# Kernel tuning notes

Measured on AMD Instinct MI355X. Metric: run time of the kernel, lower is better.

The kernel has to match this reference:

```python
import jax, jax.numpy as jnp
import numpy as np
from jax import lax

# geomloss SamplesLoss('sinkhorn', p=2, blur=0.01, scaling=0.9) semantics:
# debiased Sinkhorn divergence S_eps(a,b) = OT_eps(x,y) - 0.5*OT_eps(x,x) - 0.5*OT_eps(y,y)
# with cost C = ||x-y||^2 / 2, uniform weights, and epsilon annealing from
# diameter^p down to blur^p with ratio scaling^p.
P = 2
BLUR = 0.01
SCALING = 0.9
DIAMETER = 8.0  # static upper bound on point-cloud spread for randn data

def _eps_schedule():
    scales = []
    s = DIAMETER
    while s > BLUR:
        scales.append(s)
        s *= SCALING
    scales.append(BLUR)
    return jnp.asarray(np.array(scales, np.float32) ** P)

def _sqcost(x, y):
    # x: [B,N,D], y: [B,M,D] -> C[B,N,M] = 0.5*||x_i-y_j||^2
    x2 = jnp.sum(x * x, -1)[:, :, None]
    y2 = jnp.sum(y * y, -1)[:, None, :]
    return 0.5 * (x2 + y2 - 2.0 * jnp.einsum('bnd,bmd->bnm', x, y))

def _sinkhorn_divergence(x, y):
    B, N, _ = x.shape
    M = y.shape[1]
    logN = jnp.log(jnp.float32(N))
    logM = jnp.log(jnp.float32(M))
    eps_list = _eps_schedule()

    Cxy = _sqcost(x, y)          # [B,N,M]
    Cyx = jnp.swapaxes(Cxy, 1, 2)
    Cxx = _sqcost(x, x)
    Cyy = _sqcost(y, y)

    def softmin(eps, C, h, logw):
        # -eps * log sum_j exp(log w_j + (h_j - C_ij)/eps)
        return -eps * jax.nn.logsumexp((h[:, None, :] - C) / eps - logw, axis=-1)

    # potentials computed under envelope theorem (no grad through iterations)
    Cxy_d, Cyx_d = lax.stop_gradient(Cxy), lax.stop_gradient(Cyx)
    Cxx_d, Cyy_d = lax.stop_gradient(Cxx), lax.stop_gradient(Cyy)

    z = jnp.zeros((B, N), x.dtype)
    zy = jnp.zeros((B, M), x.dtype)

    def body(carry, eps):
        f, g, fx, gy = carry
        ft = softmin(eps, Cxy_d, g, logM)
        gt = softmin(eps, Cyx_d, f, logN)
        f, g = 0.5 * (f + ft), 0.5 * (g + gt)
        fx = 0.5 * (fx + softmin(eps, Cxx_d, fx, logN))
        gy = 0.5 * (gy + softmin(eps, Cyy_d, gy, logM))
        return (f, g, fx, gy), None

    (f, g, fx, gy), _ = lax.scan(body, (z, zy, z, zy), eps_list)

    # last extrapolation at target eps, differentiable w.r.t. the costs
    eps_t = eps_list[-1]
    f_fin = softmin(eps_t, Cxy, lax.stop_gradient(g), logM)
    g_fin = softmin(eps_t, Cyx, lax.stop_gradient(f), logN)
    fx_fin = softmin(eps_t, Cxx, lax.stop_gradient(fx), logN)
    gy_fin = softmin(eps_t, Cyy, lax.stop_gradient(gy), logM)

    # S = <a, f - fx> + <b, g - gy>, uniform weights
    return jnp.mean(f_fin - fx_fin, axis=-1) + jnp.mean(g_fin - gy_fin, axis=-1)  # [B]


def setup_inputs() -> dict:
    key = jax.random.key(0)
    k1, k2 = jax.random.split(key)
    B, N, D = 8, 2048, 3
    p1 = jax.random.normal(k1, (B, N, D), dtype=jnp.float32)
    p2 = jax.random.normal(k2, (B, N, D), dtype=jnp.float32)
    return {"p1": p1, "p2": p2}


def reference(p1, p2):
    # EMD_Loss.forward: mean over batch of per-sample Sinkhorn divergences
    return jnp.mean(_sinkhorn_divergence(p1, p2))
```

## Files before the change

kernel.cpp:

```cpp
#include <hip/hip_runtime.h>
#include <math.h>

#define NPTS 2048
#define NB 8
#define R 4
#define NW 16
#define CCH 128

typedef float v2f __attribute__((ext_vector_type(2)));

__device__ __forceinline__ float wexp2(float v) { return __builtin_amdgcn_exp2f(v); }
__device__ __forceinline__ v2f fma2(v2f a, v2f b, v2f c) {
  return __builtin_elementwise_fma(a, b, c);
}
__device__ __forceinline__ v2f max2(v2f a, v2f b) {
  return __builtin_elementwise_max(a, b);
}

__global__ __launch_bounds__(256) void emd_init(const float* __restrict__ x,
                                                const float* __restrict__ y,
                                                float4* __restrict__ x4,
                                                float4* __restrict__ y4,
                                                float* __restrict__ pot0,
                                                float* __restrict__ out) {
  int t = blockIdx.x * blockDim.x + threadIdx.x;
  if (t < NB * NPTS) {
    float a0 = x[3 * t], a1 = x[3 * t + 1], a2 = x[3 * t + 2];
    x4[t] = make_float4(a0, a1, a2, 0.5f * (a0 * a0 + a1 * a1 + a2 * a2));
    float b0 = y[3 * t], b1 = y[3 * t + 1], b2 = y[3 * t + 2];
    y4[t] = make_float4(b0, b1, b2, 0.5f * (b0 * b0 + b1 * b1 + b2 * b2));
  }
  pot0[t] = 0.0f;
  if (t == 0) out[0] = 0.0f;
}

template <bool FINAL>
__global__ __launch_bounds__(1024, 4) void emd_sweep(const float4* __restrict__ x4,
                                                     const float4* __restrict__ y4,
                                                     const float* __restrict__ pot_in,
                                                     float* __restrict__ pot_out,
                                                     float* __restrict__ out,
                                                     float c,
                                                     float neg_eps_ln2,
                                                     float eps_logM) {
  __shared__ union {
    struct {
      float4 A[NPTS / 2];
      float4 B[NPTS / 2];
    } cp;
    struct {
      float m[NW][256];
      float l[NW][256];
    } mg;
  } sh;

  int blk = blockIdx.x;
  int mat = blk >> 6;
  int b = (blk >> 3) & 7;
  int rg = blk & 7;
  int tid = threadIdx.x;
  int lane = tid & 63;
  int w = tid >> 6;

  const float4* rowp = (mat == 1 || mat == 3) ? y4 : x4;
  const float4* colp = (mat == 0 || mat == 3) ? y4 : x4;
  int hidx = (mat < 2) ? (mat ^ 1) : mat;
  const float* h = pot_in + (hidx * NB + b) * NPTS;
  const float4* colb = colp + b * NPTS;

  {
    float4 q0 = colb[2 * tid];
    float4 q1 = colb[2 * tid + 1];
    float2 hv = ((const float2*)h)[tid];
    sh.cp.A[tid] = make_float4(q0.x, q1.x, q0.y, q1.y);
    sh.cp.B[tid] = make_float4(q0.z, q1.z, (hv.x - q0.w) * c, (hv.y - q1.w) * c);
  }
  __syncthreads();

  int rowbase = rg * 256;
  const float4* rowb = rowp + b * NPTS + rowbase;

  v2f xs0[R], xs1[R], xs2[R];
  float m[R], l[R];
#pragma unroll
  for (int r = 0; r < R; ++r) {
    float4 p = rowb[r * 64 + lane];
    float a0 = p.x * c, a1 = p.y * c, a2 = p.z * c;
    xs0[r] = (v2f){a0, a0};
    xs1[r] = (v2f){a1, a1};
    xs2[r] = (v2f){a2, a2};
    m[r] = -INFINITY;
    l[r] = 0.0f;
  }

  int p0 = w * (CCH / 2);
  for (int tp = 0; tp < CCH / 2; tp += 4) {
    float4 A[4], B[4];
#pragma unroll
    for (int j = 0; j < 4; ++j) {
      A[j] = sh.cp.A[p0 + tp + j];
      B[j] = sh.cp.B[p0 + tp + j];
    }
#pragma unroll
    for (int r = 0; r < R; ++r) {
      v2f s2[4];
#pragma unroll
      for (int j = 0; j < 4; ++j) {
        v2f qx = {A[j].x, A[j].y};
        v2f qy = {A[j].z, A[j].w};
        v2f qz = {B[j].x, B[j].y};
        v2f qw = {B[j].z, B[j].w};
        s2[j] = fma2(xs0[r], qx, fma2(xs1[r], qy, fma2(xs2[r], qz, qw)));
      }
      v2f t0 = max2(s2[0], s2[1]);
      v2f t1 = max2(s2[2], s2[3]);
      v2f u = max2(t0, t1);
      float mt = fmaxf(u.x, u.y);
      float mn = fmaxf(m[r], mt);
      v2f mn2 = {mn, mn};
      v2f acc = {0.0f, 0.0f};
#pragma unroll
      for (int j = 0; j < 4; ++j) {
        v2f d = s2[j] - mn2;
        v2f e;
        e.x = wexp2(d.x);
        e.y = wexp2(d.y);
        acc += e;
      }
      float er = wexp2(m[r] - mn);
      l[r] = fmaf(l[r], er, acc.x + acc.y);
      m[r] = mn;
    }
  }

  __syncthreads();
#pragma unroll
  for (int r = 0; r < R; ++r) {
    sh.mg.m[w][r * 64 + lane] = m[r];
    sh.mg.l[w][r * 64 + lane] = l[r];
  }
  __syncthreads();

  if (w < 4) {
    int row = w * 64 + lane;
    float M = sh.mg.m[0][row];
#pragma unroll
    for (int q = 1; q < NW; ++q) M = fmaxf(M, sh.mg.m[q][row]);
    float L = 0.0f;
#pragma unroll
    for (int q = 0; q < NW; ++q)
      L += sh.mg.l[q][row] * wexp2(sh.mg.m[q][row] - M);
    float pw = rowb[row].w;
    float res = pw + neg_eps_ln2 * (M + log2f(L)) + eps_logM;
    if (FINAL) {
      float sign = (mat < 2) ? 1.0f : -1.0f;
      float val = sign * res * (1.0f / (float)(NB * NPTS));
#pragma unroll
      for (int off = 32; off; off >>= 1) val += __shfl_xor(val, off);
      if (lane == 0) atomicAdd(out, val);
    } else {
      const float* oldp = pot_in + (mat * NB + b) * NPTS + rowbase;
      float* outp = pot_out + (mat * NB + b) * NPTS + rowbase;
      outp[row] = 0.5f * (oldp[row] + res);
    }
  }
}

extern "C" void kernel_launch(void* const* d_in, const int* in_sizes, int n_in,
                              void* d_out, int out_size, void* d_ws, size_t ws_size,
                              hipStream_t stream) {
  const float* x = (const float*)d_in[0];
  const float* y = (const float*)d_in[1];
  float* out = (float*)d_out;

  char* ws = (char*)d_ws;
  float4* x4 = (float4*)ws;
  float4* y4 = (float4*)(ws + 262144);
  float* pot = (float*)(ws + 524288);

  emd_init<<<256, 256, 0, stream>>>(x, y, x4, y4, pot, out);

  float eps_arr[80];
  int ne = 0;
  double s = 8.0;
  while (s > 0.01) {
    float sf = (float)s;
    eps_arr[ne++] = sf * sf;
    s *= 0.9;
  }
  {
    float bf = 0.01f;
    eps_arr[ne++] = bf * bf;
  }

  const double LOG2E = 1.4426950408889634;
  const double LN2 = 0.6931471805599453;
  const double LOG2048 = 7.624618986159398;

  int cur = 0;
  for (int k = 0; k < ne; ++k) {
    float eps = eps_arr[k];
    float c = (float)(LOG2E / (double)eps);
    float nel = (float)(-(double)eps * LN2);
    float elM = (float)((double)eps * LOG2048);
    emd_sweep<false><<<256, 1024, 0, stream>>>(x4, y4, pot + cur * 65536,
                                               pot + (1 - cur) * 65536, out,
                                               c, nel, elM);
    cur ^= 1;
  }

  {
    float eps = eps_arr[ne - 1];
    float c = (float)(LOG2E / (double)eps);
    float nel = (float)(-(double)eps * LN2);
    float elM = (float)((double)eps * LOG2048);
    emd_sweep<true><<<256, 1024, 0, stream>>>(x4, y4, pot + cur * 65536,
                                              nullptr, out, c, nel, elM);
  }
}
```

Before: 1.704 ms.

## Replace online-max logsumexp with a reference shift carried from the previous iteration

The sweep kernel used to track a running max per row and rescale the accumulator with an extra exp every chunk. The new kernels skip that. The first iteration stores each row's max, and every later iteration stores its own log-sum-exp per row. The next iteration reads that value as a fixed shift, so the inner loop becomes just FMA, exp2 and add, with no max reductions or rescaling. The catch is numerical: if the potentials or epsilon move far enough between annealing steps, exp2 can overflow or underflow. The amax buffer is also read and written in place through pointers marked __restrict__.

```diff
diff --git a/kernel.cpp b/kernel.cpp
--- a/kernel.cpp
+++ b/kernel.cpp
@@ -34,15 +34,10 @@
   if (t == 0) out[0] = 0.0f;
 }
 
-template <bool FINAL>
-__global__ __launch_bounds__(1024, 4) void emd_sweep(const float4* __restrict__ x4,
-                                                     const float4* __restrict__ y4,
-                                                     const float* __restrict__ pot_in,
-                                                     float* __restrict__ pot_out,
-                                                     float* __restrict__ out,
-                                                     float c,
-                                                     float neg_eps_ln2,
-                                                     float eps_logM) {
+__global__ __launch_bounds__(1024, 4) void emd_sweep_boot(
+    const float4* __restrict__ x4, const float4* __restrict__ y4,
+    const float* __restrict__ pot_in, float* __restrict__ pot_out,
+    float* __restrict__ amax_out, float c, float neg_eps_ln2, float eps_logM) {
   __shared__ union {
     struct {
       float4 A[NPTS / 2];
@@ -152,6 +147,110 @@
       L += sh.mg.l[q][row] * wexp2(sh.mg.m[q][row] - M);
     float pw = rowb[row].w;
     float res = pw + neg_eps_ln2 * (M + log2f(L)) + eps_logM;
+    float invc = -neg_eps_ln2;
+    amax_out[(mat * NB + b) * NPTS + rowbase + row] = M * invc;
+    const float* oldp = pot_in + (mat * NB + b) * NPTS + rowbase;
+    float* outp = pot_out + (mat * NB + b) * NPTS + rowbase;
+    outp[row] = 0.5f * (oldp[row] + res);
+  }
+}
+
+template <bool FINAL>
+__global__ __launch_bounds__(1024, 4) void emd_sweep_ref(
+    const float4* __restrict__ x4, const float4* __restrict__ y4,
+    const float* __restrict__ pot_in, float* __restrict__ pot_out,
+    const float* __restrict__ amax_in, float* __restrict__ amax_out,
+    float* __restrict__ out, float c, float neg_eps_ln2, float eps_logM) {
+  __shared__ union {
+    struct {
+      float4 A[NPTS / 2];
+      float4 B[NPTS / 2];
+    } cp;
+    float lbuf[NW][256];
+  } sh;
+
+  int blk = blockIdx.x;
+  int mat = blk >> 6;
+  int b = (blk >> 3) & 7;
+  int rg = blk & 7;
+  int tid = threadIdx.x;
+  int lane = tid & 63;
+  int w = tid >> 6;
+
+  const float4* rowp = (mat == 1 || mat == 3) ? y4 : x4;
+  const float4* colp = (mat == 0 || mat == 3) ? y4 : x4;
+  int hidx = (mat < 2) ? (mat ^ 1) : mat;
+  const float* h = pot_in + (hidx * NB + b) * NPTS;
+  const float4* colb = colp + b * NPTS;
+
+  {
+    float4 q0 = colb[2 * tid];
+    float4 q1 = colb[2 * tid + 1];
+    float2 hv = ((const float2*)h)[tid];
+    sh.cp.A[tid] = make_float4(q0.x, q1.x, q0.y, q1.y);
+    sh.cp.B[tid] = make_float4(q0.z, q1.z, (hv.x - q0.w) * c, (hv.y - q1.w) * c);
+  }
+
+  int rowbase = rg * 256;
+  const float4* rowb = rowp + b * NPTS + rowbase;
+  const float* amrow = amax_in + (mat * NB + b) * NPTS + rowbase;
+
+  v2f xs0[R], xs1[R], xs2[R], mref2[R], acc[R];
+#pragma unroll
+  for (int r = 0; r < R; ++r) {
+    float4 p = rowb[r * 64 + lane];
+    float a0 = p.x * c, a1 = p.y * c, a2 = p.z * c;
+    xs0[r] = (v2f){a0, a0};
+    xs1[r] = (v2f){a1, a1};
+    xs2[r] = (v2f){a2, a2};
+    float mr = amrow[r * 64 + lane] * c;
+    mref2[r] = (v2f){mr, mr};
+    acc[r] = (v2f){0.0f, 0.0f};
+  }
+  __syncthreads();
+
+  int p0 = w * (CCH / 2);
+  for (int tp = 0; tp < CCH / 2; tp += 4) {
+    float4 A[4], B[4];
+#pragma unroll
+    for (int j = 0; j < 4; ++j) {
+      A[j] = sh.cp.A[p0 + tp + j];
+      B[j] = sh.cp.B[p0 + tp + j];
+    }
+#pragma unroll
+    for (int r = 0; r < R; ++r) {
+#pragma unroll
+      for (int j = 0; j < 4; ++j) {
+        v2f qx = {A[j].x, A[j].y};
+        v2f qy = {A[j].z, A[j].w};
+        v2f qz = {B[j].x, B[j].y};
+        v2f qw = {B[j].z, B[j].w};
+        v2f s2 = fma2(xs0[r], qx, fma2(xs1[r], qy, fma2(xs2[r], qz, qw)));
+        v2f d = s2 - mref2[r];
+        v2f e;
+        e.x = wexp2(d.x);
+        e.y = wexp2(d.y);
+        acc[r] += e;
+      }
+    }
+  }
+
+  __syncthreads();
+#pragma unroll
+  for (int r = 0; r < R; ++r)
+    sh.lbuf[w][r * 64 + lane] = acc[r].x + acc[r].y;
+  __syncthreads();
+
+  if (w < 4) {
+    int row = w * 64 + lane;
+    float L = sh.lbuf[0][row];
+#pragma unroll
+    for (int q = 1; q < NW; ++q) L += sh.lbuf[q][row];
+    float mr = amrow[row] * c;
+    float lse = mr + log2f(L);
+    float pw = rowb[row].w;
+    float res = pw + neg_eps_ln2 * lse + eps_logM;
+    float invc = -neg_eps_ln2;
     if (FINAL) {
       float sign = (mat < 2) ? 1.0f : -1.0f;
       float val = sign * res * (1.0f / (float)(NB * NPTS));
@@ -159,6 +258,7 @@
       for (int off = 32; off; off >>= 1) val += __shfl_xor(val, off);
       if (lane == 0) atomicAdd(out, val);
     } else {
+      amax_out[(mat * NB + b) * NPTS + rowbase + row] = lse * invc;
       const float* oldp = pot_in + (mat * NB + b) * NPTS + rowbase;
       float* outp = pot_out + (mat * NB + b) * NPTS + rowbase;
       outp[row] = 0.5f * (oldp[row] + res);
@@ -177,6 +277,7 @@
   float4* x4 = (float4*)ws;
   float4* y4 = (float4*)(ws + 262144);
   float* pot = (float*)(ws + 524288);
+  float* amax = (float*)(ws + 1048576);
 
   emd_init<<<256, 256, 0, stream>>>(x, y, x4, y4, pot, out);
 
@@ -203,9 +304,15 @@
     float c = (float)(LOG2E / (double)eps);
     float nel = (float)(-(double)eps * LN2);
     float elM = (float)((double)eps * LOG2048);
-    emd_sweep<false><<<256, 1024, 0, stream>>>(x4, y4, pot + cur * 65536,
-                                               pot + (1 - cur) * 65536, out,
+    if (k == 0) {
+      emd_sweep_boot<<<256, 1024, 0, stream>>>(x4, y4, pot + cur * 65536,
+                                               pot + (1 - cur) * 65536, amax,
                                                c, nel, elM);
+    } else {
+      emd_sweep_ref<false><<<256, 1024, 0, stream>>>(
+          x4, y4, pot + cur * 65536, pot + (1 - cur) * 65536, amax, amax, out,
+          c, nel, elM);
+    }
     cur ^= 1;
   }
 
@@ -214,7 +321,7 @@
     float c = (float)(LOG2E / (double)eps);
     float nel = (float)(-(double)eps * LN2);
     float elM = (float)((double)eps * LOG2048);
-    emd_sweep<true><<<256, 1024, 0, stream>>>(x4, y4, pot + cur * 65536,
-                                              nullptr, out, c, nel, elM);
-  }
-}
+    emd_sweep_ref<true><<<256, 1024, 0, stream>>>(
+        x4, y4, pot + cur * 65536, nullptr, amax, nullptr, out, c, nel, elM);
+  }
+}
```

Result: faster. 1.439 ms (-15.6%).
